# Optimization experiments

Measured on AMD Instinct MI355X. Metric: run time of the kernel, lower is better.

Reference implementation:

```python
import jax, jax.numpy as jnp
import numpy as np

B, S, D = 16, 4096, 64
N_HASHES, BUCKET_SIZE = 8, 64
TOKEN_SELF_ATTN_VALUE = -50000.0


def setup_inputs() -> dict:
    key = jax.random.key(0)
    k1, k2, k3 = jax.random.split(key, 3)
    qk = jax.random.normal(k1, (B, S, D), jnp.float32)
    v = jax.random.normal(k2, (B, S, D), jnp.float32)
    # random rotations for LSH hashing: (batch, dim, n_hashes, n_buckets//2)
    rotations = jax.random.normal(k3, (B, D, N_HASHES, (S // BUCKET_SIZE) // 2), jnp.float32)
    return {"qk": qk, "v": v, "rotations": rotations}


def _look_one_back(x):
    # concat each chunk with the previous chunk (wrapping): (b, c, n, ...) -> (b, c, 2n, ...)
    return jnp.concatenate([x, jnp.roll(x, 1, axis=1)], axis=2)


def _lsh_attention(qk, v, rotations):
    b, s, d = qk.shape
    n_buckets = s // BUCKET_SIZE
    # --- hash vectors (rehash_each_round=True path) ---
    rotated = jnp.einsum('btf,bfhi->bhti', qk, rotations)          # (b, h, s, nb/2)
    rotated = jnp.concatenate([rotated, -rotated], axis=-1)        # (b, h, s, nb)
    buckets = jnp.argmax(rotated, axis=-1)                          # (b, h, s)
    offsets = (jnp.arange(N_HASHES) * n_buckets)[None, :, None]
    buckets = (buckets + offsets).reshape(b, -1)                    # (b, h*s)
    # --- stable bucket sort of tokens ---
    ticker = jnp.arange(N_HASHES * s)[None, :]
    buckets_and_t = s * buckets + ticker % s
    sticker = jnp.argsort(buckets_and_t, axis=-1)                   # sorted order
    undo_sort = jnp.argsort(sticker, axis=-1)
    st = sticker % s                                                # original token index
    sqk = jnp.take_along_axis(qk, st[..., None], axis=1)            # (b, h*s, d)
    sv = jnp.take_along_axis(v, st[..., None], axis=1)
    chunk_size = N_HASHES * n_buckets
    bq_t = st.reshape(b, chunk_size, -1)                            # (b, c, n)
    bqk = sqk.reshape(b, chunk_size, -1, d)                         # (b, c, n, d)
    bv = sv.reshape(b, chunk_size, -1, d)
    # shared-QK: keys are L2-normalized queries
    norm = jnp.linalg.norm(bqk, axis=-1, keepdims=True)
    bk = bqk / jnp.maximum(norm, 1e-12)
    bk = _look_one_back(bk)                                         # (b, c, 2n, d)
    bvl = _look_one_back(bv)
    bkv_t = _look_one_back(bq_t)                                    # (b, c, 2n)
    dots = jnp.einsum('bhie,bhje->bhij', bqk, bk) * (d ** -0.5)     # (b, c, n, 2n)
    # mask self-attention (token attends to itself only as last resort)
    self_mask = bq_t[:, :, :, None] == bkv_t[:, :, None, :]
    dots = jnp.where(self_mask, TOKEN_SELF_ATTN_VALUE, dots)
    # stable softmax per chunk; keep logsumexp for cross-round combination
    lse = jax.nn.logsumexp(dots, axis=-1, keepdims=True)            # (b, c, n, 1)
    p = jnp.exp(dots - lse)
    bo = jnp.einsum('buij,buje->buie', p, bvl)                      # (b, c, n, d)
    so = bo.reshape(b, -1, d)                                       # (b, h*s, d)
    slogits = lse.reshape(b, -1)                                    # (b, h*s)
    # undo the sort
    o = jnp.take_along_axis(so, undo_sort[..., None], axis=1)
    logits = jnp.take_along_axis(slogits, undo_sort, axis=1)
    o = o.reshape(b, N_HASHES, s, d)
    logits = logits.reshape(b, N_HASHES, s, 1)
    # combine hash rounds weighted by softmax over per-round logsumexp
    probs = jnp.exp(logits - jax.nn.logsumexp(logits, axis=1, keepdims=True))
    return jnp.sum(o * probs, axis=1)                               # (b, s, d)


def reference(qk, v, rotations):
    return _lsh_attention(qk, v, rotations)
```

## Files before the change

kernel.cpp:

```cpp
#include <hip/hip_runtime.h>
#include <math.h>

#define NB_B 16
#define NB_S 4096
#define NB_D 64
#define NB_H 8

#define KSTR 72
#define PSTR 136
#define VSTR 72

typedef _Float16 half_t;
typedef __attribute__((ext_vector_type(2))) _Float16 half2t;
typedef __attribute__((ext_vector_type(4))) _Float16 half4;
typedef __attribute__((ext_vector_type(8))) _Float16 half8;
typedef __attribute__((ext_vector_type(4))) float floatx4;
typedef __attribute__((ext_vector_type(2))) float float2v;

__global__ __launch_bounds__(256) void prep_kernel(const float* __restrict__ qk,
                                                   const float* __restrict__ v,
                                                   half_t* __restrict__ khat,
                                                   half_t* __restrict__ vh,
                                                   float* __restrict__ norm) {
  int g = blockIdx.x * 256 + threadIdx.x;
  float4 qv = ((const float4*)qk)[g];
  float4 vv = ((const float4*)v)[g];
  float ss = qv.x * qv.x + qv.y * qv.y + qv.z * qv.z + qv.w * qv.w;
  for (int off = 1; off < 16; off <<= 1) ss += __shfl_xor(ss, off);
  float nr = fmaxf(sqrtf(ss), 1e-12f);
  float sc = 1.0f / nr;
  half4 hk = {(half_t)(qv.x * sc), (half_t)(qv.y * sc), (half_t)(qv.z * sc),
              (half_t)(qv.w * sc)};
  half4 hv = {(half_t)vv.x, (half_t)vv.y, (half_t)vv.z, (half_t)vv.w};
  ((half4*)khat)[g] = hk;
  ((half4*)vh)[g] = hv;
  if ((threadIdx.x & 15) == 0) norm[g >> 4] = nr;
}

__global__ __launch_bounds__(256, 1) void hash_kernel(const float* __restrict__ qk,
                                                      const float* __restrict__ rot,
                                                      int* __restrict__ bkt) {
  __shared__ float rotS[2 * 2048];
  int tid = threadIdx.x;
  int blk = blockIdx.x;
  int tile = blk & 7;
  int bhp = blk >> 3;
  int hp = bhp & 3, b = bhp >> 2;

  for (int i = tid; i < 4096; i += 256) {
    int hh = i >> 11, r = i & 2047;
    int f = r >> 5, ii = r & 31;
    rotS[i] = rot[(((size_t)b * 64 + f) * 8 + (hp * 2 + hh)) * 32 + ii];
  }
  __syncthreads();

  int t0 = (tile << 9) + tid;
  const float* qb = qk + (((size_t)b << 12) << 6);

#pragma unroll 1
  for (int hh = 0; hh < 2; hh++) {
    const float* rS = rotS + hh * 2048;
    int h = hp * 2 + hh;

    float2v acc2[2][16];
#pragma unroll
    for (int tok = 0; tok < 2; tok++)
#pragma unroll
      for (int i = 0; i < 16; i++) acc2[tok][i] = (float2v){0.f, 0.f};

#pragma unroll 1
    for (int fc = 0; fc < 8; fc++) {
      float q[2][8];
#pragma unroll
      for (int tok = 0; tok < 2; tok++) {
        const float4* qr =
            (const float4*)(qb + ((size_t)(t0 + (tok << 8)) << 6) + fc * 8);
        *(float4*)(q[tok]) = qr[0];
        *(float4*)(q[tok] + 4) = qr[1];
      }
#pragma unroll
      for (int fi = 0; fi < 8; fi++) {
#pragma unroll
        for (int i4 = 0; i4 < 8; i4++) {
          float4 wv = *(const float4*)(rS + (fc * 8 + fi) * 32 + i4 * 4);
          float2v w0 = {wv.x, wv.y};
          float2v w1 = {wv.z, wv.w};
#pragma unroll
          for (int tok = 0; tok < 2; tok++) {
            float2v q2 = {q[tok][fi], q[tok][fi]};
            float2v p0, p1;
            asm("v_pk_mul_f32 %0, %2, %3\n\t"
                "v_pk_add_f32 %1, %1, %0"
                : "=&v"(p0), "+v"(acc2[tok][i4 * 2])
                : "v"(q2), "v"(w0));
            asm("v_pk_mul_f32 %0, %2, %3\n\t"
                "v_pk_add_f32 %1, %1, %0"
                : "=&v"(p1), "+v"(acc2[tok][i4 * 2 + 1])
                : "v"(q2), "v"(w1));
          }
        }
      }
    }

#pragma unroll
    for (int tok = 0; tok < 2; tok++) {
      float a[32];
#pragma unroll
      for (int p = 0; p < 16; p++) {
        a[2 * p] = acc2[tok][p].x;
        a[2 * p + 1] = acc2[tok][p].y;
      }
      float b1 = a[0];
      int i1 = 0;
#pragma unroll
      for (int i = 1; i < 32; i++)
        if (a[i] > b1) { b1 = a[i]; i1 = i; }
#pragma unroll
      for (int i = 0; i < 32; i++) {
        float x = -a[i];
        if (x > b1) { b1 = x; i1 = 32 + i; }
      }
      bkt[(((size_t)(b * 8 + h)) << 12) + t0 + (tok << 8)] = i1;
    }
  }
}

__global__ __launch_bounds__(1024) void sort_kernel(const int* __restrict__ bkt,
                                                    int* __restrict__ st) {
  __shared__ int lb[4096];
  __shared__ int hist[4096];
  __shared__ int cumoff[64];
  int tid = threadIdx.x;
  int b = blockIdx.x >> 3, h = blockIdx.x & 7;
  const int* gb = bkt + (((size_t)(b * 8 + h)) << 12);
  for (int t = tid; t < 4096; t += 1024) lb[t] = gb[t];
  for (int i = tid; i < 4096; i += 1024) hist[i] = 0;
  __syncthreads();
  for (int t = tid; t < 4096; t += 1024) atomicAdd(&hist[((t >> 6) << 6) | lb[t]], 1);
  __syncthreads();
  if (tid < 64) {
    int run = 0;
    for (int cc = 0; cc < 64; cc++) {
      int x = hist[(cc << 6) | tid];
      hist[(cc << 6) | tid] = run;
      run += x;
    }
    int s = run;
    for (int off = 1; off < 64; off <<= 1) {
      int u = __shfl_up(s, off);
      if (tid >= off) s += u;
    }
    cumoff[tid] = s - run;
  }
  __syncthreads();
  int lane = tid & 63;
  for (int p = 0; p < 4; p++) {
    int t = (p << 10) + tid;
    int vb = lb[t];
    unsigned long long m = 0xFFFFFFFFFFFFFFFFull;
#pragma unroll
    for (int bit = 0; bit < 6; bit++) {
      unsigned long long bl = __ballot((vb >> bit) & 1);
      m &= ((vb >> bit) & 1) ? bl : ~bl;
    }
    int rank = __popcll(m & ((1ull << lane) - 1ull));
    int cpos = cumoff[vb] + hist[((t >> 6) << 6) | vb] + rank;
    st[(((size_t)(b * 8 + h)) << 12) + cpos] = t;
  }
}

#define MASK2 -72134.76f
__global__ __launch_bounds__(256) void chunk_kernel(const half_t* __restrict__ khat,
                                                    const half_t* __restrict__ vh,
                                                    const float* __restrict__ norm,
                                                    const int* __restrict__ st,
                                                    half_t* __restrict__ oh,
                                                    float* __restrict__ lse) {
  __shared__ __align__(16) half_t Ks[128 * KSTR];
  __shared__ __align__(16) half_t Vt0[64 * VSTR];
  __shared__ __align__(16) half_t Vt1[64 * VSTR];
  __shared__ int tk[128];
  __shared__ float normS[64];
  int tid = threadIdx.x;
  int b = blockIdx.x & 15;
  int g = blockIdx.x >> 4;
  int h = g >> 6, c = g & 63;
  int gp = (g + 511) & 511;
  int hp = gp >> 6, cp = gp & 63;
  if (tid < 64) {
    tk[tid] = st[(((size_t)(b * 8 + h)) << 12) + (c << 6) + tid];
  } else if (tid < 128) {
    tk[tid] = st[(((size_t)(b * 8 + hp)) << 12) + (cp << 6) + (tid - 64)];
  }
  __syncthreads();
  if (tid < 64) normS[tid] = norm[(b << 12) + tk[tid]];
  for (int idx = tid; idx < 1024; idx += 256) {
    int row = idx >> 3, fo = idx & 7;
    half8 val = *(const half8*)(khat + (((size_t)(b << 12) + tk[row]) << 6) + fo * 8);
    *(half8*)(Ks + row * KSTR + fo * 8) = val;
  }
  {
    int kp = tid & 31, ch = tid >> 5;
    half8 r0 = *(const half8*)(vh + (((size_t)(b << 12) + tk[2 * kp]) << 6) + ch * 8);
    half8 r1 = *(const half8*)(vh + (((size_t)(b << 12) + tk[2 * kp + 1]) << 6) + ch * 8);
    half8 r2 = *(const half8*)(vh + (((size_t)(b << 12) + tk[64 + 2 * kp]) << 6) + ch * 8);
    half8 r3 = *(const half8*)(vh + (((size_t)(b << 12) + tk[65 + 2 * kp]) << 6) + ch * 8);
#pragma unroll
    for (int j = 0; j < 8; j++) {
      half2t p0 = {r0[j], r1[j]};
      half2t p1 = {r2[j], r3[j]};
      *(half2t*)(Vt0 + (ch * 8 + j) * VSTR + 2 * kp) = p0;
      *(half2t*)(Vt1 + (ch * 8 + j) * VSTR + 2 * kp) = p1;
    }
  }
  __syncthreads();

  int lane = tid & 63, w = tid >> 6;
  int m = lane & 15, quad = lane >> 4;
  half8 afr[2];
#pragma unroll
  for (int ki = 0; ki < 2; ki++)
    afr[ki] = *(const half8*)(Ks + (w * 16 + m) * KSTR + ki * 32 + quad * 8);
  bool c0 = (c == 0);
  float scr[4];
#pragma unroll
  for (int r = 0; r < 4; r++) {
    int rr = w * 16 + quad * 4 + r;
    scr[r] = 0.18033688f * normS[rr];
  }
  int ti[4] = {0, 0, 0, 0};
  if (c0) {
#pragma unroll
    for (int r = 0; r < 4; r++) ti[r] = tk[w * 16 + quad * 4 + r];
  }

  float d[8][4];
#pragma unroll
  for (int nt = 0; nt < 8; nt++) {
    floatx4 acc = {0.f, 0.f, 0.f, 0.f};
#pragma unroll
    for (int ki = 0; ki < 2; ki++) {
      half8 bfr = *(const half8*)(Ks + (nt * 16 + m) * KSTR + ki * 32 + quad * 8);
      acc = __builtin_amdgcn_mfma_f32_16x16x32_f16(afr[ki], bfr, acc, 0, 0, 0);
    }
    if (nt < 4) {
      if (nt == w) {
#pragma unroll
        for (int r = 0; r < 4; r++)
          d[nt][r] = (m == quad * 4 + r) ? MASK2 : acc[r] * scr[r];
      } else {
#pragma unroll
        for (int r = 0; r < 4; r++) d[nt][r] = acc[r] * scr[r];
      }
    } else {
      if (c0) {
        int tj = tk[nt * 16 + m];
#pragma unroll
        for (int r = 0; r < 4; r++)
          d[nt][r] = (ti[r] == tj) ? MASK2 : acc[r] * scr[r];
      } else {
#pragma unroll
        for (int r = 0; r < 4; r++) d[nt][r] = acc[r] * scr[r];
      }
    }
  }

  float mr4[4], lr4[4];
#pragma unroll
  for (int r = 0; r < 4; r++) {
    float mm = d[0][r];
#pragma unroll
    for (int nt = 1; nt < 8; nt++) mm = fmaxf(mm, d[nt][r]);
    for (int off = 1; off < 16; off <<= 1) mm = fmaxf(mm, __shfl_xor(mm, off));
    mr4[r] = mm;
  }
#pragma unroll
  for (int nt = 0; nt < 8; nt++)
#pragma unroll
    for (int r = 0; r < 4; r++)
      d[nt][r] = __builtin_amdgcn_exp2f(d[nt][r] - mr4[r]);
#pragma unroll
  for (int r = 0; r < 4; r++) {
    float ll = 0.f;
#pragma unroll
    for (int nt = 0; nt < 8; nt++) ll += d[nt][r];
    for (int off = 1; off < 16; off <<= 1) ll += __shfl_xor(ll, off);
    lr4[r] = ll;
    if (m == 0) {
      int rr = w * 16 + quad * 4 + r;
      lse[(((size_t)(b * 8 + h)) << 12) + tk[rr]] =
          0.69314718f * (mr4[r] + __builtin_amdgcn_logf(ll));
    }
  }
  __syncthreads();

  half_t* Ps = Ks;
#pragma unroll
  for (int nt = 0; nt < 8; nt++) {
#pragma unroll
    for (int r = 0; r < 4; r++) {
      Ps[(w * 16 + quad * 4 + r) * PSTR + nt * 16 + m] = (half_t)d[nt][r];
    }
  }

  half8 pfr[4];
#pragma unroll
  for (int kk = 0; kk < 4; kk++)
    pfr[kk] = *(const half8*)(Ps + (w * 16 + m) * PSTR + kk * 32 + quad * 8);

  floatx4 accO[4];
#pragma unroll
  for (int dt = 0; dt < 4; dt++) accO[dt] = (floatx4){0.f, 0.f, 0.f, 0.f};

#pragma unroll
  for (int dt = 0; dt < 4; dt++) {
#pragma unroll
    for (int kk = 0; kk < 2; kk++) {
      half8 bfr = *(const half8*)(Vt0 + (dt * 16 + m) * VSTR + kk * 32 + quad * 8);
      accO[dt] = __builtin_amdgcn_mfma_f32_16x16x32_f16(pfr[kk], bfr, accO[dt], 0, 0, 0);
    }
#pragma unroll
    for (int kk = 2; kk < 4; kk++) {
      half8 bfr = *(const half8*)(Vt1 + (dt * 16 + m) * VSTR + (kk - 2) * 32 + quad * 8);
      accO[dt] = __builtin_amdgcn_mfma_f32_16x16x32_f16(pfr[kk], bfr, accO[dt], 0, 0, 0);
    }
  }
  __syncthreads();

  half_t* Ot = Vt0;
#pragma unroll
  for (int r = 0; r < 4; r++) {
    float inv = 1.0f / lr4[r];
#pragma unroll
    for (int dt = 0; dt < 4; dt++) {
      Ot[(w * 16 + quad * 4 + r) * VSTR + dt * 16 + m] = (half_t)(accO[dt][r] * inv);
    }
  }
  __syncthreads();
  for (int idx = tid; idx < 512; idx += 256) {
    int row = idx >> 3, fo = idx & 7;
    half8 val = *(const half8*)(Ot + row * VSTR + fo * 8);
    *(half8*)(oh + ((((size_t)(b * 8 + h)) << 12) + tk[row]) * 64 + fo * 8) = val;
  }
}

__global__ __launch_bounds__(256) void combine_kernel(const half_t* __restrict__ oh,
                                                      const float* __restrict__ lse,
                                                      float* __restrict__ out) {
  int idx = blockIdx.x * 256 + threadIdx.x;
  int do8 = idx & 7;
  int ts = idx >> 3;
  int b = ts >> 12, t = ts & 4095;
  size_t base = ((size_t)b << 15) + t;
  float L[8];
  float m = -3.4e38f;
#pragma unroll
  for (int h = 0; h < 8; h++) {
    L[h] = lse[base + ((size_t)h << 12)];
    m = fmaxf(m, L[h]);
  }
  float s = 0.f;
#pragma unroll
  for (int h = 0; h < 8; h++) s += __expf(L[h] - m);
  float lt = m + __logf(s);
  float acc[8];
#pragma unroll
  for (int j = 0; j < 8; j++) acc[j] = 0.f;
#pragma unroll
  for (int h = 0; h < 8; h++) {
    float wgt = __expf(L[h] - lt);
    half8 o = *(const half8*)(oh + ((base + ((size_t)h << 12)) << 6) + do8 * 8);
#pragma unroll
    for (int j = 0; j < 8; j++) acc[j] += wgt * (float)o[j];
  }
  float* dst = out + ((((size_t)b << 12) + t) << 6) + do8 * 8;
  *(float4*)dst = (float4){acc[0], acc[1], acc[2], acc[3]};
  *(float4*)(dst + 4) = (float4){acc[4], acc[5], acc[6], acc[7]};
}

extern "C" void kernel_launch(void* const* d_in, const int* in_sizes, int n_in,
                              void* d_out, int out_size, void* d_ws, size_t ws_size,
                              hipStream_t stream) {
  const float* qk = (const float*)d_in[0];
  const float* v = (const float*)d_in[1];
  const float* rot = (const float*)d_in[2];
  float* out = (float*)d_out;

  int* bkt = (int*)d_ws;
  int* stp = bkt + NB_B * NB_H * NB_S;
  float* lse = (float*)(stp + NB_B * NB_H * NB_S);
  float* norm = lse + NB_B * NB_H * NB_S;
  half_t* khat = (half_t*)(norm + NB_B * NB_S);
  half_t* vh = khat + (size_t)NB_B * NB_S * NB_D;
  half_t* oh = vh + (size_t)NB_B * NB_S * NB_D;

  prep_kernel<<<NB_B * NB_S * 16 / 256, 256, 0, stream>>>(qk, v, khat, vh, norm);
  hash_kernel<<<NB_B * 4 * 8, 256, 0, stream>>>(qk, rot, bkt);
  sort_kernel<<<NB_B * NB_H, 1024, 0, stream>>>(bkt, stp);
  chunk_kernel<<<NB_B * 512, 256, 0, stream>>>(khat, vh, norm, stp, oh, lse);
  combine_kernel<<<NB_B * NB_S * 8 / 256, 256, 0, stream>>>(oh, lse, out);
}
```

Baseline: 210.3 us.

## Split hash argmax across lanes and double hash kernel grid

The hash kernel is remapped so that each thread computes 4 of the 32 rotation columns for 8 tokens and both hash rounds together. The argmax is then finished with cross-lane shuffles. The grid doubles to 1024 blocks, with each thread handling fewer accumulators, which aims to raise parallelism and occupancy for the hashing stage. This adds shuffle reductions, a tie-break rule on lowest index, and qk loads that are less coalesced because each thread reads 8 consecutive token rows.

```diff
diff --git a/kernel.cpp b/kernel.cpp
--- a/kernel.cpp
+++ b/kernel.cpp
@@ -43,8 +43,8 @@
   __shared__ float rotS[2 * 2048];
   int tid = threadIdx.x;
   int blk = blockIdx.x;
-  int tile = blk & 7;
-  int bhp = blk >> 3;
+  int tile = blk & 15;
+  int bhp = blk >> 4;
   int hp = bhp & 3, b = bhp >> 2;
 
   for (int i = tid; i < 4096; i += 256) {
@@ -54,73 +54,101 @@
   }
   __syncthreads();
 
-  int t0 = (tile << 9) + tid;
+  int lane = tid & 63, w = tid >> 6;
+  int s = lane & 7, gi = lane >> 3;
+  int t0 = (tile << 8) + (w << 6) + (s << 3);
   const float* qb = qk + (((size_t)b << 12) << 6);
 
+  float2v accA[8][2], accB[8][2];
+#pragma unroll
+  for (int k = 0; k < 8; k++) {
+    accA[k][0] = (float2v){0.f, 0.f};
+    accA[k][1] = (float2v){0.f, 0.f};
+    accB[k][0] = (float2v){0.f, 0.f};
+    accB[k][1] = (float2v){0.f, 0.f};
+  }
+
 #pragma unroll 1
-  for (int hh = 0; hh < 2; hh++) {
-    const float* rS = rotS + hh * 2048;
-    int h = hp * 2 + hh;
-
-    float2v acc2[2][16];
-#pragma unroll
-    for (int tok = 0; tok < 2; tok++)
-#pragma unroll
-      for (int i = 0; i < 16; i++) acc2[tok][i] = (float2v){0.f, 0.f};
-
-#pragma unroll 1
-    for (int fc = 0; fc < 8; fc++) {
-      float q[2][8];
-#pragma unroll
-      for (int tok = 0; tok < 2; tok++) {
-        const float4* qr =
-            (const float4*)(qb + ((size_t)(t0 + (tok << 8)) << 6) + fc * 8);
-        *(float4*)(q[tok]) = qr[0];
-        *(float4*)(q[tok] + 4) = qr[1];
-      }
-#pragma unroll
-      for (int fi = 0; fi < 8; fi++) {
-#pragma unroll
-        for (int i4 = 0; i4 < 8; i4++) {
-          float4 wv = *(const float4*)(rS + (fc * 8 + fi) * 32 + i4 * 4);
-          float2v w0 = {wv.x, wv.y};
-          float2v w1 = {wv.z, wv.w};
-#pragma unroll
-          for (int tok = 0; tok < 2; tok++) {
-            float2v q2 = {q[tok][fi], q[tok][fi]};
-            float2v p0, p1;
-            asm("v_pk_mul_f32 %0, %2, %3\n\t"
-                "v_pk_add_f32 %1, %1, %0"
-                : "=&v"(p0), "+v"(acc2[tok][i4 * 2])
-                : "v"(q2), "v"(w0));
-            asm("v_pk_mul_f32 %0, %2, %3\n\t"
-                "v_pk_add_f32 %1, %1, %0"
-                : "=&v"(p1), "+v"(acc2[tok][i4 * 2 + 1])
-                : "v"(q2), "v"(w1));
-          }
-        }
-      }
-    }
-
-#pragma unroll
-    for (int tok = 0; tok < 2; tok++) {
-      float a[32];
-#pragma unroll
-      for (int p = 0; p < 16; p++) {
-        a[2 * p] = acc2[tok][p].x;
-        a[2 * p + 1] = acc2[tok][p].y;
-      }
-      float b1 = a[0];
-      int i1 = 0;
-#pragma unroll
-      for (int i = 1; i < 32; i++)
-        if (a[i] > b1) { b1 = a[i]; i1 = i; }
-#pragma unroll
-      for (int i = 0; i < 32; i++) {
-        float x = -a[i];
-        if (x > b1) { b1 = x; i1 = 32 + i; }
-      }
-      bkt[(((size_t)(b * 8 + h)) << 12) + t0 + (tok << 8)] = i1;
+  for (int fq = 0; fq < 16; fq++) {
+    float q4[8][4];
+#pragma unroll
+    for (int k = 0; k < 8; k++)
+      *(float4*)(q4[k]) =
+          *(const float4*)(qb + ((size_t)(t0 + k) << 6) + fq * 4);
+#pragma unroll
+    for (int fi = 0; fi < 4; fi++) {
+      float4 wa = *(const float4*)(rotS + (fq * 4 + fi) * 32 + gi * 4);
+      float4 wb = *(const float4*)(rotS + 2048 + (fq * 4 + fi) * 32 + gi * 4);
+      float2v wa0 = {wa.x, wa.y}, wa1 = {wa.z, wa.w};
+      float2v wb0 = {wb.x, wb.y}, wb1 = {wb.z, wb.w};
+#pragma unroll
+      for (int k = 0; k < 8; k++) {
+        float2v q2 = {q4[k][fi], q4[k][fi]};
+        float2v p0, p1, p2, p3;
+        asm("v_pk_mul_f32 %0, %2, %3\n\t"
+            "v_pk_add_f32 %1, %1, %0"
+            : "=&v"(p0), "+v"(accA[k][0])
+            : "v"(q2), "v"(wa0));
+        asm("v_pk_mul_f32 %0, %2, %3\n\t"
+            "v_pk_add_f32 %1, %1, %0"
+            : "=&v"(p1), "+v"(accA[k][1])
+            : "v"(q2), "v"(wa1));
+        asm("v_pk_mul_f32 %0, %2, %3\n\t"
+            "v_pk_add_f32 %1, %1, %0"
+            : "=&v"(p2), "+v"(accB[k][0])
+            : "v"(q2), "v"(wb0));
+        asm("v_pk_mul_f32 %0, %2, %3\n\t"
+            "v_pk_add_f32 %1, %1, %0"
+            : "=&v"(p3), "+v"(accB[k][1])
+            : "v"(q2), "v"(wb1));
+      }
+    }
+  }
+
+  int gb4 = gi * 4;
+  size_t baseA = ((size_t)(b * 8 + hp * 2)) << 12;
+  size_t baseB = ((size_t)(b * 8 + hp * 2 + 1)) << 12;
+#pragma unroll
+  for (int k = 0; k < 8; k++) {
+    {
+      float a[4] = {accA[k][0].x, accA[k][0].y, accA[k][1].x, accA[k][1].y};
+      float bv = a[0];
+      int bi = gb4;
+#pragma unroll
+      for (int j = 1; j < 4; j++)
+        if (a[j] > bv) { bv = a[j]; bi = gb4 + j; }
+#pragma unroll
+      for (int j = 0; j < 4; j++) {
+        float x = -a[j];
+        if (x > bv) { bv = x; bi = 32 + gb4 + j; }
+      }
+#pragma unroll
+      for (int off = 8; off < 64; off <<= 1) {
+        float ov = __shfl_xor(bv, off);
+        int oi = __shfl_xor(bi, off);
+        if (ov > bv || (ov == bv && oi < bi)) { bv = ov; bi = oi; }
+      }
+      if (gi == 0) bkt[baseA + t0 + k] = bi;
+    }
+    {
+      float a[4] = {accB[k][0].x, accB[k][0].y, accB[k][1].x, accB[k][1].y};
+      float bv = a[0];
+      int bi = gb4;
+#pragma unroll
+      for (int j = 1; j < 4; j++)
+        if (a[j] > bv) { bv = a[j]; bi = gb4 + j; }
+#pragma unroll
+      for (int j = 0; j < 4; j++) {
+        float x = -a[j];
+        if (x > bv) { bv = x; bi = 32 + gb4 + j; }
+      }
+#pragma unroll
+      for (int off = 8; off < 64; off <<= 1) {
+        float ov = __shfl_xor(bv, off);
+        int oi = __shfl_xor(bi, off);
+        if (ov > bv || (ov == bv && oi < bi)) { bv = ov; bi = oi; }
+      }
+      if (gi == 0) bkt[baseB + t0 + k] = bi;
     }
   }
 }
@@ -395,7 +423,7 @@
   half_t* oh = vh + (size_t)NB_B * NB_S * NB_D;
 
   prep_kernel<<<NB_B * NB_S * 16 / 256, 256, 0, stream>>>(qk, v, khat, vh, norm);
-  hash_kernel<<<NB_B * 4 * 8, 256, 0, stream>>>(qk, rot, bkt);
+  hash_kernel<<<NB_B * 4 * 16, 256, 0, stream>>>(qk, rot, bkt);
   sort_kernel<<<NB_B * NB_H, 1024, 0, stream>>>(bkt, stp);
   chunk_kernel<<<NB_B * 512, 256, 0, stream>>>(khat, vh, norm, stp, oh, lse);
   combine_kernel<<<NB_B * NB_S * 8 / 256, 256, 0, stream>>>(oh, lse, out);
```

After: 233.3 us. 1.11x slower.
